# Kernel tuning notes

Hardware: AMD Instinct MI355X
Metric: run time of the kernel (lower is better)

## Reference

```python
import jax, jax.numpy as jnp
import numpy as np

NUM_NODES = 20000
NUM_EDGES = 1_000_000
NUM_REL = 12        # internal num_relation (init arg 24 // 2)
NUM_STEP = 6
HID = 128
B_SET = 64          # number of unique (h, r) queries
BS, NEG = 64, 32    # scoring batch
EPS = 1e-10


def setup_inputs() -> dict:
    key = jax.random.key(0)
    ks = jax.random.split(key, 16)
    s = 0.1
    inp = {
        "query_emb": jax.random.normal(ks[0], (2 * NUM_REL + 1, HID), jnp.float32) * s,
        "w_ih": jax.random.normal(ks[1], (4 * HID, HID), jnp.float32) * s,
        "w_hh": jax.random.normal(ks[2], (4 * HID, HID), jnp.float32) * s,
        "b_ih": jax.random.normal(ks[3], (4 * HID,), jnp.float32) * s,
        "b_hh": jax.random.normal(ks[4], (4 * HID,), jnp.float32) * s,
        "wl_w": jax.random.normal(ks[5], (2 * NUM_REL, HID), jnp.float32) * s,
        "wl_b": jax.random.normal(ks[6], (2 * NUM_REL,), jnp.float32) * s,
        "lin_w": jax.random.normal(ks[7], (1, 1), jnp.float32),
        "lin_b": jax.random.normal(ks[8], (1,), jnp.float32),
        "edge_index": jax.random.randint(ks[9], (2, NUM_EDGES), 0, NUM_NODES, jnp.int64),
        "edge_type": jax.random.randint(ks[10], (NUM_EDGES,), 0, 2 * NUM_REL, jnp.int64),
        "h_set": jax.random.randint(ks[11], (B_SET,), 0, NUM_NODES, jnp.int64),
        "r_set": jax.random.randint(ks[12], (B_SET,), 0, NUM_REL, jnp.int64),
        "t_index": jax.random.randint(ks[13], (BS, NEG), 0, NUM_NODES, jnp.int64),
        "hr_inverse": jax.random.randint(ks[14], (BS, NEG), 0, B_SET, jnp.int64),
    }
    return inp


def _lstm(query, w_ih, w_hh, b_ih, b_hh):
    # query: [T, B, D]; single-layer PyTorch LSTM (gate order i, f, g, o)
    B, D = query.shape[1], w_hh.shape[1]
    h0 = jnp.zeros((B, D), query.dtype)

    def step(carry, x):
        h, c = carry
        gates = x @ w_ih.T + b_ih + h @ w_hh.T + b_hh
        i, f, g, o = jnp.split(gates, 4, axis=-1)
        c = jax.nn.sigmoid(f) * c + jax.nn.sigmoid(i) * jnp.tanh(g)
        h = jax.nn.sigmoid(o) * jnp.tanh(c)
        return (h, c), h

    _, hidden = jax.lax.scan(step, (h0, h0), query)
    return hidden  # [T, B, D]


def reference(query_emb, w_ih, w_hh, b_ih, b_hh, wl_w, wl_b, lin_w, lin_b,
              edge_index, edge_type, h_set, r_set, t_index, hr_inverse):
    N1 = NUM_NODES + 1
    B = h_set.shape[0]
    # query sequence: relation repeated (T-1) times, then END token (= NUM_REL)
    q_index = jnp.concatenate(
        [jnp.tile(r_set[None, :], (NUM_STEP - 1, 1)),
         jnp.full((1, B), NUM_REL, dtype=r_set.dtype)], axis=0)  # [T, B]
    query = query_emb[q_index]                                   # [T, B, D]
    hidden = _lstm(query, w_ih, w_hh, b_ih, b_hh)                # [T, B, D]

    memory = jax.nn.one_hot(h_set, N1, dtype=query_emb.dtype)[None]  # [1, B, N1]
    node_in, node_out = edge_index[0], edge_index[1]

    output = None
    for i in range(NUM_STEP):
        k = hidden[i]                 # [B, D]
        v = hidden[: i + 1]           # [i+1, B, D]
        attn = jax.nn.softmax(jnp.einsum('bd,tbd->bt', k, v), axis=-1)
        inp = jnp.einsum('bt,tbn->nb', attn, memory)             # [N1, B]
        weight = jax.nn.softmax(k @ wl_w.T + wl_b, axis=-1).T    # [2R, B]
        # gather -> weight -> scatter_add over edges (edge_weight == 1)
        message = inp[node_in] * weight[edge_type]               # [E, B]
        output = jax.ops.segment_sum(message, node_out, num_segments=N1)
        output = output / jnp.maximum(output.sum(0, keepdims=True), EPS)
        memory = jnp.concatenate([memory, output.T[None]], axis=0)

    score = output[t_index, hr_inverse]           # [BS, NEG]
    return score * lin_w[0, 0] + lin_b[0]
```

## Files before the change

kernel.cpp:

```cpp
#include <hip/hip_runtime.h>
#include <hip/hip_fp16.h>
#include <math.h>

namespace {

constexpr int kN1 = 20001;
constexpr int kNE = 1000000;
constexpr int kNStep = 6;
constexpr int kHid = 128;
constexpr int kB = 64;
constexpr int kNRel2 = 24;
constexpr float kEps = 1e-10f;
constexpr unsigned kSent = (unsigned)kN1;
constexpr int kPMax = kNE + 8 * kN1;
constexpr int kGatherBlocks = 2048;
constexpr int kNWaves = kGatherBlocks * 4;
constexpr int kNXcd = 8;

__device__ __forceinline__ float sig(float x) { return 1.0f / (1.0f + expf(-x)); }

__device__ __forceinline__ float2 cvt2(unsigned u) {
  __half2 h = *reinterpret_cast<__half2*>(&u);
  return __half22float2(h);
}


__global__ __launch_bounds__(256) void transpose_w_kernel(
    const float* __restrict__ w_ih, const float* __restrict__ w_hh,
    float* __restrict__ wt) {
  const int idx = blockIdx.x * 256 + threadIdx.x;
  if (idx < 256 * 512) {
    const int k = idx >> 9;
    const int j = idx & 511;
    wt[idx] = (k < 128) ? w_ih[j * kHid + k] : w_hh[j * kHid + (k - 128)];
  }
}

__global__ __launch_bounds__(512) void lstm_fast_kernel(
    const float* __restrict__ query_emb, const float* __restrict__ wt,
    const float* __restrict__ b_ih, const float* __restrict__ b_hh,
    const int* __restrict__ r_set, float* __restrict__ hidden ) {
  const int b = blockIdx.x;
  const int tid = threadIdx.x;
  __shared__ float xh[256];
  __shared__ float cst[kHid];
  __shared__ float gsm[512];
  const float bias = b_ih[tid] + b_hh[tid];
  const int q = r_set[b];
  if (tid < kHid) { cst[tid] = 0.f; xh[kHid + tid] = 0.f; }
  for (int s = 0; s < kNStep; ++s) {
    if (tid < kHid) xh[tid] = query_emb[((s < kNStep - 1) ? q : 12) * kHid + tid];
    __syncthreads();
    float acc = bias;
#pragma unroll 8
    for (int k = 0; k < 256; ++k) acc += xh[k] * wt[k * 512 + tid];
    gsm[tid] = acc;
    __syncthreads();
    if (tid < kHid) {
      const float ig = sig(gsm[tid]);
      const float fg = sig(gsm[kHid + tid]);
      const float gg = tanhf(gsm[2 * kHid + tid]);
      const float og = sig(gsm[3 * kHid + tid]);
      const float cn = fg * cst[tid] + ig * gg;
      cst[tid] = cn;
      const float hn = og * tanhf(cn);
      xh[kHid + tid] = hn;
      hidden[(s * kB + b) * kHid + tid] = hn;
    }
    __syncthreads();
  }
}

__global__ __launch_bounds__(256) void lstm_kernel(
    const float* __restrict__ query_emb, const float* __restrict__ w_ih,
    const float* __restrict__ w_hh, const float* __restrict__ b_ih,
    const float* __restrict__ b_hh, const int* __restrict__ r_set,
    float* __restrict__ hidden) {
  const int b = blockIdx.x;
  const int tid = threadIdx.x;
  __shared__ float xs[kHid], hs[kHid], cs[kHid], gates[4 * kHid];
  if (tid < kHid) { hs[tid] = 0.f; cs[tid] = 0.f; }
  __syncthreads();
  for (int s = 0; s < kNStep; ++s) {
    const int q = (s < kNStep - 1) ? r_set[b] : 12;
    if (tid < kHid) xs[tid] = query_emb[q * kHid + tid];
    __syncthreads();
    for (int j = tid; j < 4 * kHid; j += blockDim.x) {
      const float* wi = &w_ih[j * kHid];
      const float* wh = &w_hh[j * kHid];
      float a = b_ih[j] + b_hh[j];
#pragma unroll 4
      for (int k = 0; k < kHid; ++k) a += xs[k] * wi[k] + hs[k] * wh[k];
      gates[j] = a;
    }
    __syncthreads();
    if (tid < kHid) {
      const float ig = sig(gates[tid]);
      const float fg = sig(gates[kHid + tid]);
      const float gg = tanhf(gates[2 * kHid + tid]);
      const float og = sig(gates[3 * kHid + tid]);
      const float cn = fg * cs[tid] + ig * gg;
      const float hn = og * tanhf(cn);
      cs[tid] = cn;
      hs[tid] = hn;
      hidden[(s * kB + b) * kHid + tid] = hn;
    }
    __syncthreads();
  }
}

__global__ __launch_bounds__(128) void attn_weight_kernel(
    const float* __restrict__ hidden, const float* __restrict__ wl_w,
    const float* __restrict__ wl_b, float* __restrict__ attnAll ,
    float* __restrict__ weightAll ) {
  const int b = blockIdx.x;
  const int tid = threadIdx.x;
  __shared__ float hsm[kNStep][kHid];
  __shared__ float G[kNStep][kNStep];
  __shared__ float logits[kNStep][kNRel2];
  for (int s = 0; s < kNStep; ++s) hsm[s][tid] = hidden[(s * kB + b) * kHid + tid];
  __syncthreads();
  if (tid < 36) {
    const int i = tid / 6, t = tid % 6;
    if (t <= i) {
      float acc = 0.f;
      for (int k = 0; k < kHid; ++k) acc += hsm[i][k] * hsm[t][k];
      G[i][t] = acc;
    }
  }
  for (int p = tid; p < kNStep * kNRel2; p += 128) {
    const int i = p / kNRel2, r = p % kNRel2;
    float acc = wl_b[r];
    for (int k = 0; k < kHid; ++k) acc += hsm[i][k] * wl_w[r * kHid + k];
    logits[i][r] = acc;
  }
  __syncthreads();
  if (tid < kNStep) {
    const int i = tid;
    float m = G[i][0];
    for (int t = 1; t <= i; ++t) m = fmaxf(m, G[i][t]);
    float ssum = 0.f;
    float ev[kNStep];
    for (int t = 0; t <= i; ++t) { ev[t] = expf(G[i][t] - m); ssum += ev[t]; }
    for (int t = 0; t <= i; ++t) attnAll[(i * kNStep + t) * kB + b] = ev[t] / ssum;
    float mw = logits[i][0];
    for (int r = 1; r < kNRel2; ++r) mw = fmaxf(mw, logits[i][r]);
    float sw = 0.f;
    float ew[kNRel2];
    for (int r = 0; r < kNRel2; ++r) { ew[r] = expf(logits[i][r] - mw); sw += ew[r]; }
    for (int r = 0; r < kNRel2; ++r) weightAll[(i * kNRel2 + r) * kB + b] = ew[r] / sw;
  }
}


__global__ __launch_bounds__(256) void zero_kernel(int* __restrict__ count2,
                                                   float* __restrict__ colsumAll) {
  const int i = blockIdx.x * blockDim.x + threadIdx.x;
  if (i < kN1 * kNXcd) count2[i] = 0;
  if (i < kNStep * kB) colsumAll[i] = 0.f;
}

__global__ __launch_bounds__(256) void hist2_kernel(const int* __restrict__ nout,
                                                    int* __restrict__ count2) {
  const int xcd = blockIdx.x & (kNXcd - 1);
  for (int e = blockIdx.x * blockDim.x + threadIdx.x; e < kNE;
       e += gridDim.x * blockDim.x)
    atomicAdd(&count2[nout[e] * kNXcd + xcd], 1);
}

__global__ __launch_bounds__(1024) void scan_kernel(int* __restrict__ count2,
                                                    int* __restrict__ counts,
                                                    int* __restrict__ poffsets) {
  __shared__ int part[1024];
  const int tid = threadIdx.x;
  const int chunk = (kN1 + 1023) / 1024;
  const int beg = tid * chunk;
  const int end = min(beg + chunk, kN1);
  int s = 0;
  for (int i = beg; i < end; ++i) {
    int c = 0;
#pragma unroll
    for (int x = 0; x < kNXcd; ++x) c += count2[i * kNXcd + x];
    counts[i] = c;
    s += (c + 7) & ~7;
  }
  part[tid] = s;
  __syncthreads();
  for (int off = 1; off < 1024; off <<= 1) {
    const int v = (tid >= off) ? part[tid - off] : 0;
    __syncthreads();
    part[tid] += v;
    __syncthreads();
  }
  int run = part[tid] - s;
  for (int i = beg; i < end; ++i) {
    poffsets[i] = run;
    int sub = run;
#pragma unroll
    for (int x = 0; x < kNXcd; ++x) {
      const int c = count2[i * kNXcd + x];
      count2[i * kNXcd + x] = sub;
      sub += c;
    }
    run += (counts[i] + 7) & ~7;
  }
  if (tid == 1023) poffsets[kN1] = part[1023];
}

__global__ __launch_bounds__(256) void pad_fill_kernel(
    const int* __restrict__ poffsets, const int* __restrict__ counts,
    unsigned* __restrict__ packed) {
  const int i = blockIdx.x * blockDim.x + threadIdx.x;
  if (i < kN1) {
    const int s = poffsets[i] + counts[i];
    const int e = poffsets[i + 1];
    for (int k = s; k < e; ++k) packed[k] = kSent;
  }
}

__global__ __launch_bounds__(256) void permute_kernel(
    const int* __restrict__ nin, const int* __restrict__ nout,
    const int* __restrict__ etype, int* __restrict__ cursor2,
    unsigned* __restrict__ packed) {
  const int xcd = blockIdx.x & (kNXcd - 1);
  for (int e = blockIdx.x * blockDim.x + threadIdx.x; e < kNE;
       e += gridDim.x * blockDim.x) {
    const int d = nout[e];
    const int pos = atomicAdd(&cursor2[d * kNXcd + xcd], 1);
    packed[pos] = (unsigned)nin[e] | ((unsigned)etype[e] << 15);
  }
}


__global__ __launch_bounds__(256) void inp_kernel(
    const float* __restrict__ attnAll, const float* __restrict__ colsumAll,
    const int* __restrict__ h_set, const float* __restrict__ outs,
    __half* __restrict__ inp, int step) {
  __shared__ float coef[kNStep][kB];
  __shared__ int hsm[kB];
  const int tid = threadIdx.x;
  for (int j = tid; j < kNStep * kB; j += 256) {
    const int t = j >> 6, b = j & 63;
    float c = 0.f;
    if (t == 0)
      c = attnAll[(step * kNStep) * kB + b];
    else if (t <= step)
      c = attnAll[(step * kNStep + t) * kB + b] /
          fmaxf(colsumAll[(t - 1) * kB + b], kEps);
    coef[t][b] = c;
  }
  if (tid < kB) hsm[tid] = h_set[tid];
  __syncthreads();
  const int total = (kN1 + 1) * 16;
  for (int idx = blockIdx.x * blockDim.x + tid; idx < total;
       idx += gridDim.x * blockDim.x) {
    const int n = idx >> 4;
    const int cg = idx & 15;
    float ax = 0.f, ay = 0.f, az = 0.f, aw = 0.f;
    if (n < kN1) {
      for (int t = 1; t <= step; ++t) {
        const float4 ct = *reinterpret_cast<const float4*>(&coef[t][cg * 4]);
        const float4 o = *reinterpret_cast<const float4*>(
            &outs[((long long)(t - 1) * kN1 + n) * kB + cg * 4]);
        ax += ct.x * o.x; ay += ct.y * o.y; az += ct.z * o.z; aw += ct.w * o.w;
      }
      const int c0 = cg * 4;
      if (hsm[c0 + 0] == n) ax += coef[0][c0 + 0];
      if (hsm[c0 + 1] == n) ay += coef[0][c0 + 1];
      if (hsm[c0 + 2] == n) az += coef[0][c0 + 2];
      if (hsm[c0 + 3] == n) aw += coef[0][c0 + 3];
    }
    __half2 h0 = __floats2half2_rn(ax, ay);
    __half2 h1 = __floats2half2_rn(az, aw);
    uint2 u;
    u.x = *reinterpret_cast<unsigned*>(&h0);
    u.y = *reinterpret_cast<unsigned*>(&h1);
    *reinterpret_cast<uint2*>(inp + (long long)idx * 4) = u;
  }
}

__global__ __launch_bounds__(256) void gather_seg_kernel(
    const __half* __restrict__ inp ,
    const float* __restrict__ weight ,
    const unsigned* __restrict__ packed, const int* __restrict__ poffsets,
    float* __restrict__ out, float* __restrict__ colsum) {
  __shared__ __align__(16) __half wsm[kNRel2 * kB];
  __shared__ float red[4][kB];
  const int tid = threadIdx.x;
  const int lane = tid & 63;
  const int wid = tid >> 6;
  const int g = lane >> 3;
  const int cb = lane & 7;
  {
    const uint4* base = reinterpret_cast<const uint4*>(inp);
    const int tot = (kN1 + 1) * 8;
    const int per = (tot + 255) / 256;
    const int s0 = (blockIdx.x & 255) * per;
    const int s1 = min(s0 + per, tot);
    unsigned sink = 0;
    for (int i = s0 + tid; i < s1; i += 256) sink ^= base[i].x;
    asm volatile("" :: "v"(sink));
  }
  for (int j = tid; j < kNRel2 * kB; j += 256) wsm[j] = __float2half(weight[j]);
  __syncthreads();

  float csum[8] = {0.f, 0.f, 0.f, 0.f, 0.f, 0.f, 0.f, 0.f};
  float acc[8] = {0.f, 0.f, 0.f, 0.f, 0.f, 0.f, 0.f, 0.f};

  auto flushNode = [&](int node) {
#pragma unroll
    for (int j = 0; j < 8; ++j) {
      acc[j] += __shfl_xor(acc[j], 8);
      acc[j] += __shfl_xor(acc[j], 16);
      acc[j] += __shfl_xor(acc[j], 32);
    }
    if (g == 0) {
      *reinterpret_cast<float4*>(out + (long long)node * kB + cb * 8) =
          make_float4(acc[0], acc[1], acc[2], acc[3]);
      *reinterpret_cast<float4*>(out + (long long)node * kB + cb * 8 + 4) =
          make_float4(acc[4], acc[5], acc[6], acc[7]);
#pragma unroll
      for (int j = 0; j < 8; ++j) csum[j] += acc[j];
    }
#pragma unroll
    for (int j = 0; j < 8; ++j) acc[j] = 0.f;
  };

  const int wave = blockIdx.x * 4 + wid;
  const int P = poffsets[kN1];
  const int nG = P >> 3;
  const int chunkG = (nG + kNWaves - 1) / kNWaves;
  const int gbeg = wave * chunkG;
  if (gbeg < nG) {
    const int gend = min(gbeg + chunkG, nG);
    auto lb = [&](int x) {
      int lo = 0, hi = kN1;
      while (lo < hi) {
        const int mid = (lo + hi) >> 1;
        if (poffsets[mid] < x) lo = mid + 1; else hi = mid;
      }
      return lo;
    };
    const int nbeg = lb(gbeg * 8);
    const int nend = (gend >= nG) ? kN1 : lb(gend * 8);
    if (nbeg < nend) {
      int n = nbeg;
      int nextB = poffsets[n + 1];
      const int ebeg = poffsets[nbeg];
      const int eend = poffsets[nend];
      auto ld_pk = [&](int idx) -> unsigned {
        const unsigned r = packed[idx];
        return (idx < eend) ? r : kSent;
      };
      auto rowload = [&](unsigned p) -> uint4 {
        return *reinterpret_cast<const uint4*>(
            inp + (long long)(p & 0x7fffu) * kB + cb * 8);
      };
      unsigned pb = ld_pk(ebeg + lane);
      unsigned p0 = __shfl(pb, g);
      unsigned p1 = __shfl(pb, 8 + g);
      uint4 v0 = rowload(p0);
      uint4 v1 = rowload(p1);
      for (int wbase = ebeg; wbase < eend; wbase += 64) {
        const unsigned pbN = ld_pk(wbase + 64 + lane);
#pragma unroll
        for (int j = 0; j < 8; ++j) {
          const int cur = wbase + j * 8;
          if (cur >= eend) break;
          const int jj = j + 2;
          const unsigned p2 = (jj < 8) ? __shfl(pb, jj * 8 + g)
                                       : __shfl(pbN, (jj - 8) * 8 + g);
          const uint4 v2 = rowload(p2);
          while (cur >= nextB) { flushNode(n); ++n; nextB = poffsets[n + 1]; }
          const uint4 w4 =
              *reinterpret_cast<const uint4*>(wsm + (p0 >> 15) * kB + cb * 8);
          const float2 a0 = cvt2(v0.x), a1 = cvt2(v0.y), a2 = cvt2(v0.z),
                       a3 = cvt2(v0.w);
          const float2 b0 = cvt2(w4.x), b1 = cvt2(w4.y), b2 = cvt2(w4.z),
                       b3 = cvt2(w4.w);
          acc[0] += a0.x * b0.x; acc[1] += a0.y * b0.y;
          acc[2] += a1.x * b1.x; acc[3] += a1.y * b1.y;
          acc[4] += a2.x * b2.x; acc[5] += a2.y * b2.y;
          acc[6] += a3.x * b3.x; acc[7] += a3.y * b3.y;
          p0 = p1; v0 = v1; p1 = p2; v1 = v2;
        }
        pb = pbN;
      }
      while (n < nend) { flushNode(n); ++n; }
    }
  }
  if (g == 0) {
#pragma unroll
    for (int j = 0; j < 8; ++j) red[wid][cb * 8 + j] = csum[j];
  }
  __syncthreads();
  if (wid == 0) {
    const float r = red[0][lane] + red[1][lane] + red[2][lane] + red[3][lane];
    unsafeAtomicAdd(&colsum[lane], r);
  }
}

__global__ __launch_bounds__(256) void score_kernel(
    const float* __restrict__ outLast, const float* __restrict__ colsumLast,
    const int* __restrict__ t_index, const int* __restrict__ hr_inverse,
    const float* __restrict__ lin_w, const float* __restrict__ lin_b,
    float* __restrict__ out, int n) {
  const int i = blockIdx.x * blockDim.x + threadIdx.x;
  if (i < n) {
    const int node = t_index[i];
    const int b = hr_inverse[i];
    const float v = outLast[(long long)node * kB + b] / fmaxf(colsumLast[b], kEps);
    out[i] = v * lin_w[0] + lin_b[0];
  }
}


__global__ __launch_bounds__(256) void inp_zero_kernel(
    const float* __restrict__ attnAll, const int* __restrict__ h_set,
    const float* __restrict__ outs, float* __restrict__ inp,
    float* __restrict__ out_next, float* __restrict__ colsum, int step) {
  const long long total = (long long)kN1 * kB;
  for (long long idx = (long long)blockIdx.x * blockDim.x + threadIdx.x; idx < total;
       idx += (long long)gridDim.x * blockDim.x) {
    const int b = (int)(idx & 63);
    const int n = (int)(idx >> 6);
    float acc = (h_set[b] == n) ? attnAll[(step * kNStep) * kB + b] : 0.f;
    for (int t = 1; t <= step; ++t)
      acc += attnAll[(step * kNStep + t) * kB + b] *
             outs[(long long)(t - 1) * kN1 * kB + idx];
    inp[idx] = acc;
    out_next[idx] = 0.f;
  }
  if (blockIdx.x == 0 && threadIdx.x < kB) colsum[threadIdx.x] = 0.f;
}

__global__ __launch_bounds__(256) void scatter_kernel(
    const float* __restrict__ inp, const float* __restrict__ weight,
    const int* __restrict__ nin, const int* __restrict__ nout,
    const int* __restrict__ etype, float* __restrict__ out,
    float* __restrict__ colsum) {
  const int lane = threadIdx.x & 63;
  const int wave = blockIdx.x * (blockDim.x >> 6) + (threadIdx.x >> 6);
  const int nwave = gridDim.x * (blockDim.x >> 6);
  __shared__ float wsm[kNRel2 * kB];
  for (int j = threadIdx.x; j < kNRel2 * kB; j += blockDim.x) wsm[j] = weight[j];
  __syncthreads();
  float csum = 0.f;
  for (int e = wave; e < kNE; e += nwave) {
    const float v = inp[(long long)nin[e] * kB + lane] * wsm[etype[e] * kB + lane];
    unsafeAtomicAdd(&out[(long long)nout[e] * kB + lane], v);
    csum += v;
  }
  unsafeAtomicAdd(&colsum[lane], csum);
}

__global__ __launch_bounds__(256) void normalize_kernel(
    float* __restrict__ out, const float* __restrict__ colsum) {
  const long long total = (long long)kN1 * kB;
  for (long long idx = (long long)blockIdx.x * blockDim.x + threadIdx.x; idx < total;
       idx += (long long)gridDim.x * blockDim.x)
    out[idx] /= fmaxf(colsum[idx & 63], kEps);
}

__global__ __launch_bounds__(256) void score_kernel_norm(
    const float* __restrict__ outLast, const int* __restrict__ t_index,
    const int* __restrict__ hr_inverse, const float* __restrict__ lin_w,
    const float* __restrict__ lin_b, float* __restrict__ out, int n) {
  const int i = blockIdx.x * blockDim.x + threadIdx.x;
  if (i < n) {
    out[i] = outLast[(long long)t_index[i] * kB + hr_inverse[i]] * lin_w[0] + lin_b[0];
  }
}

}

extern "C" void kernel_launch(void* const* d_in, const int* in_sizes, int n_in,
                              void* d_out, int out_size, void* d_ws, size_t ws_size,
                              hipStream_t stream) {
  const float* query_emb = (const float*)d_in[0];
  const float* w_ih = (const float*)d_in[1];
  const float* w_hh = (const float*)d_in[2];
  const float* b_ih = (const float*)d_in[3];
  const float* b_hh = (const float*)d_in[4];
  const float* wl_w = (const float*)d_in[5];
  const float* wl_b = (const float*)d_in[6];
  const float* lin_w = (const float*)d_in[7];
  const float* lin_b = (const float*)d_in[8];
  const int* edge_index = (const int*)d_in[9];
  const int* edge_type = (const int*)d_in[10];
  const int* h_set = (const int*)d_in[11];
  const int* r_set = (const int*)d_in[12];
  const int* t_index = (const int*)d_in[13];
  const int* hr_inverse = (const int*)d_in[14];
  float* out = (float*)d_out;

  const int* nin = edge_index;
  const int* nout = edge_index + kNE;

  float* ws = (float*)d_ws;
  float* hidden = ws;
  float* attnAll = hidden + kNStep * kB * kHid;
  float* weightAll = attnAll + kNStep * kNStep * kB;
  float* colsumAll = weightAll + kNStep * kNRel2 * kB;
  float* inpF32 = colsumAll + kNStep * kB;
  __half* inpH = (__half*)inpF32;
  float* outs = inpF32 + (long long)kN1 * kB;
  float* tail = outs + (long long)kNStep * kN1 * kB;
  int* counts = (int*)tail;
  int* poffsets = counts + kN1;
  int* count2 = poffsets + kN1 + 1;
  unsigned* packed = (unsigned*)(count2 + kN1 * kNXcd);
  float* wt = (float*)(packed + kPMax);
  const size_t needed = (size_t)((char*)(wt + 256 * 512) - (char*)d_ws);

  if (ws_size >= needed) {
    transpose_w_kernel<<<512, 256, 0, stream>>>(w_ih, w_hh, wt);
    lstm_fast_kernel<<<kB, 512, 0, stream>>>(query_emb, wt, b_ih, b_hh, r_set, hidden);
    attn_weight_kernel<<<kB, 128, 0, stream>>>(hidden, wl_w, wl_b, attnAll, weightAll);

    zero_kernel<<<(kN1 * kNXcd + 255) / 256, 256, 0, stream>>>(count2, colsumAll);
    hist2_kernel<<<1024, 256, 0, stream>>>(nout, count2);
    scan_kernel<<<1, 1024, 0, stream>>>(count2, counts, poffsets);
    pad_fill_kernel<<<(kN1 + 255) / 256, 256, 0, stream>>>(poffsets, counts, packed);
    permute_kernel<<<1024, 256, 0, stream>>>(nin, nout, edge_type, count2, packed);

    const int inp_threads = (kN1 + 1) * 16;
    for (int i = 0; i < kNStep; ++i) {
      float* out_i = outs + (long long)i * kN1 * kB;
      inp_kernel<<<(inp_threads + 255) / 256, 256, 0, stream>>>(
          attnAll, colsumAll, h_set, outs, inpH, i);
      gather_seg_kernel<<<kGatherBlocks, 256, 0, stream>>>(
          inpH, weightAll + i * kNRel2 * kB, packed, poffsets, out_i,
          colsumAll + i * kB);
    }
    score_kernel<<<(out_size + 255) / 256, 256, 0, stream>>>(
        outs + 5LL * kN1 * kB, colsumAll + 5 * kB, t_index, hr_inverse, lin_w, lin_b,
        out, out_size);
  } else {
    lstm_kernel<<<kB, 256, 0, stream>>>(query_emb, w_ih, w_hh, b_ih, b_hh, r_set,
                                        hidden);
    attn_weight_kernel<<<kB, 128, 0, stream>>>(hidden, wl_w, wl_b, attnAll, weightAll);
    float* colsum = colsumAll;
    for (int i = 0; i < kNStep; ++i) {
      float* out_i = outs + (long long)i * kN1 * kB;
      inp_zero_kernel<<<2048, 256, 0, stream>>>(attnAll, h_set, outs, inpF32, out_i,
                                                colsum, i);
      scatter_kernel<<<4096, 256, 0, stream>>>(inpF32, weightAll + i * kNRel2 * kB,
                                               nin, nout, edge_type, out_i, colsum);
      normalize_kernel<<<2048, 256, 0, stream>>>(out_i, colsum);
    }
    score_kernel_norm<<<(out_size + 255) / 256, 256, 0, stream>>>(
        outs + 5LL * kN1 * kB, t_index, hr_inverse, lin_w, lin_b, out, out_size);
  }
}
```

Before: 737.8 us.

## Parallelize CSR scan, add nontemporal loads/stores, remap gather blocks per XCD

Replaces the single-block 1024-thread prefix scan with a three-kernel multi-block scan (block reduce, block-sum scan, block-local scan and offset write), so the serial per-thread chunk loops are spread across many CUs. Also marks streaming accesses (outs reads in inp_kernel, packed edge reads, out writes in the gather) as nontemporal to keep the inp table resident in cache. Gather block indices are remapped so consecutive virtual blocks land on the same XCD, improving locality of L2 prefetch and work ranges. Adds two extra kernel launches in exchange for parallel scan work.

```diff
diff --git a/kernel.cpp b/kernel.cpp
--- a/kernel.cpp
+++ b/kernel.cpp
@@ -16,6 +16,10 @@
 constexpr int kGatherBlocks = 2048;
 constexpr int kNWaves = kGatherBlocks * 4;
 constexpr int kNXcd = 8;
+constexpr int kScanBlocks = (kN1 + 255) / 256;
+
+typedef float f32x4 __attribute__((ext_vector_type(4)));
+typedef unsigned u32x4 __attribute__((ext_vector_type(4)));
 
 __device__ __forceinline__ float sig(float x) { return 1.0f / (1.0f + expf(-x)); }
 
@@ -168,43 +172,72 @@
     atomicAdd(&count2[nout[e] * kNXcd + xcd], 1);
 }
 
-__global__ __launch_bounds__(1024) void scan_kernel(int* __restrict__ count2,
+__global__ __launch_bounds__(256) void scanA_kernel(const int* __restrict__ count2,
                                                     int* __restrict__ counts,
+                                                    int* __restrict__ blockSum) {
+  const int tid = threadIdx.x;
+  const int n = blockIdx.x * 256 + tid;
+  int padded = 0;
+  if (n < kN1) {
+    int c = 0;
+#pragma unroll
+    for (int x = 0; x < kNXcd; ++x) c += count2[n * kNXcd + x];
+    counts[n] = c;
+    padded = (c + 7) & ~7;
+  }
+  __shared__ int sm[256];
+  sm[tid] = padded;
+  __syncthreads();
+  for (int off = 128; off > 0; off >>= 1) {
+    if (tid < off) sm[tid] += sm[tid + off];
+    __syncthreads();
+  }
+  if (tid == 0) blockSum[blockIdx.x] = sm[0];
+}
+
+__global__ __launch_bounds__(128) void scanB_kernel(int* __restrict__ blockSum) {
+  const int tid = threadIdx.x;
+  __shared__ int sm[128];
+  const int v = (tid < kScanBlocks) ? blockSum[tid] : 0;
+  sm[tid] = v;
+  __syncthreads();
+  for (int off = 1; off < 128; off <<= 1) {
+    const int t = (tid >= off) ? sm[tid - off] : 0;
+    __syncthreads();
+    sm[tid] += t;
+    __syncthreads();
+  }
+  if (tid < kScanBlocks) blockSum[tid] = sm[tid] - v;
+}
+
+__global__ __launch_bounds__(256) void scanC_kernel(const int* __restrict__ counts,
+                                                    const int* __restrict__ blockSum,
+                                                    int* __restrict__ count2,
                                                     int* __restrict__ poffsets) {
-  __shared__ int part[1024];
-  const int tid = threadIdx.x;
-  const int chunk = (kN1 + 1023) / 1024;
-  const int beg = tid * chunk;
-  const int end = min(beg + chunk, kN1);
-  int s = 0;
-  for (int i = beg; i < end; ++i) {
-    int c = 0;
-#pragma unroll
-    for (int x = 0; x < kNXcd; ++x) c += count2[i * kNXcd + x];
-    counts[i] = c;
-    s += (c + 7) & ~7;
-  }
-  part[tid] = s;
-  __syncthreads();
-  for (int off = 1; off < 1024; off <<= 1) {
-    const int v = (tid >= off) ? part[tid - off] : 0;
-    __syncthreads();
-    part[tid] += v;
-    __syncthreads();
-  }
-  int run = part[tid] - s;
-  for (int i = beg; i < end; ++i) {
-    poffsets[i] = run;
-    int sub = run;
+  const int tid = threadIdx.x;
+  const int n = blockIdx.x * 256 + tid;
+  const int padded = (n < kN1) ? ((counts[n] + 7) & ~7) : 0;
+  __shared__ int sm[256];
+  sm[tid] = padded;
+  __syncthreads();
+  for (int off = 1; off < 256; off <<= 1) {
+    const int t = (tid >= off) ? sm[tid - off] : 0;
+    __syncthreads();
+    sm[tid] += t;
+    __syncthreads();
+  }
+  const int excl = sm[tid] - padded + blockSum[blockIdx.x];
+  if (n < kN1) {
+    poffsets[n] = excl;
+    int sub = excl;
 #pragma unroll
     for (int x = 0; x < kNXcd; ++x) {
-      const int c = count2[i * kNXcd + x];
-      count2[i * kNXcd + x] = sub;
+      const int c = count2[n * kNXcd + x];
+      count2[n * kNXcd + x] = sub;
       sub += c;
     }
-    run += (counts[i] + 7) & ~7;
-  }
-  if (tid == 1023) poffsets[kN1] = part[1023];
+    if (n == kN1 - 1) poffsets[kN1] = excl + padded;
+  }
 }
 
 __global__ __launch_bounds__(256) void pad_fill_kernel(
@@ -260,8 +293,8 @@
     if (n < kN1) {
       for (int t = 1; t <= step; ++t) {
         const float4 ct = *reinterpret_cast<const float4*>(&coef[t][cg * 4]);
-        const float4 o = *reinterpret_cast<const float4*>(
-            &outs[((long long)(t - 1) * kN1 + n) * kB + cg * 4]);
+        const f32x4 o = __builtin_nontemporal_load(reinterpret_cast<const f32x4*>(
+            &outs[((long long)(t - 1) * kN1 + n) * kB + cg * 4]));
         ax += ct.x * o.x; ay += ct.y * o.y; az += ct.z * o.z; aw += ct.w * o.w;
       }
       const int c0 = cg * 4;
@@ -291,11 +324,13 @@
   const int wid = tid >> 6;
   const int g = lane >> 3;
   const int cb = lane & 7;
+  const int vb = (blockIdx.x & (kNXcd - 1)) * (kGatherBlocks / kNXcd) +
+                 (blockIdx.x >> 3);
   {
-    const uint4* base = reinterpret_cast<const uint4*>(inp);
+    const u32x4* base = reinterpret_cast<const u32x4*>(inp);
     const int tot = (kN1 + 1) * 8;
     const int per = (tot + 255) / 256;
-    const int s0 = (blockIdx.x & 255) * per;
+    const int s0 = (vb & 255) * per;
     const int s1 = min(s0 + per, tot);
     unsigned sink = 0;
     for (int i = s0 + tid; i < s1; i += 256) sink ^= base[i].x;
@@ -315,10 +350,12 @@
       acc[j] += __shfl_xor(acc[j], 32);
     }
     if (g == 0) {
-      *reinterpret_cast<float4*>(out + (long long)node * kB + cb * 8) =
-          make_float4(acc[0], acc[1], acc[2], acc[3]);
-      *reinterpret_cast<float4*>(out + (long long)node * kB + cb * 8 + 4) =
-          make_float4(acc[4], acc[5], acc[6], acc[7]);
+      const f32x4 o0 = {acc[0], acc[1], acc[2], acc[3]};
+      const f32x4 o1 = {acc[4], acc[5], acc[6], acc[7]};
+      __builtin_nontemporal_store(
+          o0, reinterpret_cast<f32x4*>(out + (long long)node * kB + cb * 8));
+      __builtin_nontemporal_store(
+          o1, reinterpret_cast<f32x4*>(out + (long long)node * kB + cb * 8 + 4));
 #pragma unroll
       for (int j = 0; j < 8; ++j) csum[j] += acc[j];
     }
@@ -326,7 +363,7 @@
     for (int j = 0; j < 8; ++j) acc[j] = 0.f;
   };
 
-  const int wave = blockIdx.x * 4 + wid;
+  const int wave = vb * 4 + wid;
   const int P = poffsets[kN1];
   const int nG = P >> 3;
   const int chunkG = (nG + kNWaves - 1) / kNWaves;
@@ -349,18 +386,18 @@
       const int ebeg = poffsets[nbeg];
       const int eend = poffsets[nend];
       auto ld_pk = [&](int idx) -> unsigned {
-        const unsigned r = packed[idx];
+        const unsigned r = __builtin_nontemporal_load(packed + idx);
         return (idx < eend) ? r : kSent;
       };
-      auto rowload = [&](unsigned p) -> uint4 {
-        return *reinterpret_cast<const uint4*>(
+      auto rowload = [&](unsigned p) -> u32x4 {
+        return *reinterpret_cast<const u32x4*>(
             inp + (long long)(p & 0x7fffu) * kB + cb * 8);
       };
       unsigned pb = ld_pk(ebeg + lane);
       unsigned p0 = __shfl(pb, g);
       unsigned p1 = __shfl(pb, 8 + g);
-      uint4 v0 = rowload(p0);
-      uint4 v1 = rowload(p1);
+      u32x4 v0 = rowload(p0);
+      u32x4 v1 = rowload(p1);
       for (int wbase = ebeg; wbase < eend; wbase += 64) {
         const unsigned pbN = ld_pk(wbase + 64 + lane);
 #pragma unroll
@@ -370,10 +407,10 @@
           const int jj = j + 2;
           const unsigned p2 = (jj < 8) ? __shfl(pb, jj * 8 + g)
                                        : __shfl(pbN, (jj - 8) * 8 + g);
-          const uint4 v2 = rowload(p2);
+          const u32x4 v2 = rowload(p2);
           while (cur >= nextB) { flushNode(n); ++n; nextB = poffsets[n + 1]; }
-          const uint4 w4 =
-              *reinterpret_cast<const uint4*>(wsm + (p0 >> 15) * kB + cb * 8);
+          const u32x4 w4 =
+              *reinterpret_cast<const u32x4*>(wsm + (p0 >> 15) * kB + cb * 8);
           const float2 a0 = cvt2(v0.x), a1 = cvt2(v0.y), a2 = cvt2(v0.z),
                        a3 = cvt2(v0.w);
           const float2 b0 = cvt2(w4.x), b1 = cvt2(w4.y), b2 = cvt2(w4.z),
@@ -509,7 +546,8 @@
   int* counts = (int*)tail;
   int* poffsets = counts + kN1;
   int* count2 = poffsets + kN1 + 1;
-  unsigned* packed = (unsigned*)(count2 + kN1 * kNXcd);
+  int* blockSum = count2 + kN1 * kNXcd;
+  unsigned* packed = (unsigned*)(blockSum + 128);
   float* wt = (float*)(packed + kPMax);
   const size_t needed = (size_t)((char*)(wt + 256 * 512) - (char*)d_ws);
 
@@ -520,7 +558,9 @@
 
     zero_kernel<<<(kN1 * kNXcd + 255) / 256, 256, 0, stream>>>(count2, colsumAll);
     hist2_kernel<<<1024, 256, 0, stream>>>(nout, count2);
-    scan_kernel<<<1, 1024, 0, stream>>>(count2, counts, poffsets);
+    scanA_kernel<<<kScanBlocks, 256, 0, stream>>>(count2, counts, blockSum);
+    scanB_kernel<<<1, 128, 0, stream>>>(blockSum);
+    scanC_kernel<<<kScanBlocks, 256, 0, stream>>>(counts, blockSum, count2, poffsets);
     pad_fill_kernel<<<(kN1 + 255) / 256, 256, 0, stream>>>(poffsets, counts, packed);
     permute_kernel<<<1024, 256, 0, stream>>>(nin, nout, edge_type, count2, packed);
 
```

Result: faster. 622.8 us (-15.6%).
